# Optimization experiments

Measured on AMD Instinct MI355X. Metric: run time of the kernel, lower is better.

Reference implementation:

```python
import jax, jax.numpy as jnp
from jax import lax
import numpy as np

IN_DIM, HID, B, T = 64, 512, 256, 512


def _lstm_layer(xs, W_ih, W_hh, b_ih, b_hh):
    # xs: [B, T, D_in]; W_ih: [4H, D_in]; W_hh: [4H, H]; biases: [4H]
    Bn = xs.shape[0]
    H = W_hh.shape[1]
    # Precompute input projection for all timesteps (one big GEMM).
    x_proj = jnp.einsum('btd,gd->btg', xs, W_ih) + b_ih + b_hh  # [B, T, 4H]

    def step(carry, xp):
        h, c = carry
        g = xp + h @ W_hh.T  # [B, 4H], PyTorch gate order: i, f, g, o
        i, f, gg, o = jnp.split(g, 4, axis=-1)
        i = jax.nn.sigmoid(i)
        f = jax.nn.sigmoid(f)
        gg = jnp.tanh(gg)
        o = jax.nn.sigmoid(o)
        c = f * c + i * gg
        h = o * jnp.tanh(c)
        return (h, c), h

    z = jnp.zeros((Bn, H), xs.dtype)
    _, hs = lax.scan(step, (z, z), jnp.swapaxes(x_proj, 0, 1))  # [T, B, H]
    return jnp.swapaxes(hs, 0, 1)  # [B, T, H]


def setup_inputs() -> dict:
    key = jax.random.key(0)
    ks = jax.random.split(key, 16)
    s_in = 1.0 / np.sqrt(HID)
    u = lambda k, shp: jax.random.uniform(k, shp, jnp.float32, -s_in, s_in)
    return {
        'x': jax.random.normal(ks[0], (B, T, IN_DIM), jnp.float32),
        'W_ih0': u(ks[1], (4 * HID, IN_DIM)),
        'W_hh0': u(ks[2], (4 * HID, HID)),
        'b_ih0': u(ks[3], (4 * HID,)),
        'b_hh0': u(ks[4], (4 * HID,)),
        'W_ih1': u(ks[5], (4 * HID, HID)),
        'W_hh1': u(ks[6], (4 * HID, HID)),
        'b_ih1': u(ks[7], (4 * HID,)),
        'b_hh1': u(ks[8], (4 * HID,)),
        'W1': u(ks[9], (HID // 2, HID)),
        'b1': u(ks[10], (HID // 2,)),
        'W2': u(ks[11], (1, HID // 2)),
        'b2': u(ks[12], (1,)),
    }


def reference(x, W_ih0, W_hh0, b_ih0, b_hh0, W_ih1, W_hh1, b_ih1, b_hh1, W1, b1, W2, b2):
    h1 = _lstm_layer(x, W_ih0, W_hh0, b_ih0, b_hh0)   # [B, T, H]
    h2 = _lstm_layer(h1, W_ih1, W_hh1, b_ih1, b_hh1)  # [B, T, H] (inference: no inter-layer dropout)
    last = h2[:, -1, :]                                # final timestep
    hidden = jax.nn.relu(last @ W1.T + b1)
    return jax.nn.sigmoid(hidden @ W2.T + b2)          # [B, 1]
```

## Files before the change

### kernel.cpp

```cpp
#include <hip/hip_runtime.h>
#include <hip/hip_bf16.h>
#include <stdint.h>


#define Bsz 256
#define Tsz 512
#define IND 64
#define Hsz 512
#define BH (Bsz * Hsz)
#define FLAG_STRIDE 16

typedef __attribute__((ext_vector_type(8))) short short8;
typedef __attribute__((ext_vector_type(4))) float floatx4;

static __device__ __forceinline__ short f2bf(float f) {
    unsigned u = __float_as_uint(f);
    u += 0x7FFFu + ((u >> 16) & 1u);
    return (short)(u >> 16);
}
static __device__ __forceinline__ float bf2f(short s) {
    return __uint_as_float(((unsigned)(unsigned short)s) << 16);
}
static __device__ __forceinline__ float sigm(float z) { return 1.f / (1.f + __expf(-z)); }
static __device__ __forceinline__ float tanh_f(float z) { return 2.f / (1.f + __expf(-2.f * z)) - 1.f; }

static __device__ __forceinline__ short8 ring16(const short* p) {
    short8 v;
    asm volatile("global_load_dwordx4 %0, %1, off sc1" : "=v"(v) : "v"(p));
    return v;
}

__global__ __launch_bounds__(512, 1) void lstm_pers(
    const float* __restrict__ x,
    const float* __restrict__ Wih0, const float* __restrict__ Whh0,
    const float* __restrict__ bih0, const float* __restrict__ bhh0,
    const float* __restrict__ Wih1, const float* __restrict__ Whh1,
    const float* __restrict__ bih1, const float* __restrict__ bhh1,
    int* __restrict__ flags, short* __restrict__ h1ring, short* __restrict__ h2ring)
{
    __shared__ __align__(16) char smem[147712];
    short* w  = (short*)smem;
    float* p1 = (float*)(smem + 131072);

    const int tid = threadIdx.x;
    const int bid = blockIdx.x;
    const int layer = bid >> 7;
    const int lb    = bid & 127;
    const int grp   = lb >> 5;
    const int chunk = lb & 31;

    if (layer == 0) {
        for (int idx = tid; idx < 64 * 576; idx += 512) {
            int n = idx / 576, kc = idx - n * 576;
            int grow = (n >> 4) * Hsz + chunk * 16 + (n & 15);
            float v = (kc < IND) ? Wih0[grow * IND + kc]
                                 : Whh0[(size_t)grow * Hsz + kc - IND];
            w[n * 640 + (kc ^ ((n & 7) << 4))] = f2bf(v);
        }
    } else {
        for (int idx = tid; idx < 64 * 1024; idx += 512) {
            int n = idx >> 10, kc = idx & 1023;
            int grow = (n >> 4) * Hsz + chunk * 16 + (n & 15);
            float v = (kc < Hsz) ? Wih1[(size_t)grow * Hsz + kc]
                                 : Whh1[(size_t)grow * Hsz + kc - Hsz];
            w[n * 1024 + (kc ^ ((n & 7) << 4))] = f2bf(v);
        }
    }

    const int lane  = tid & 63;
    const int wv    = tid >> 6;
    const int mslot = wv >> 1;
    const int kh    = wv & 1;
    const int q     = lane >> 4;
    const int cl    = lane & 15;
    const int rowbase = grp * 64 + mslot * 16;
    const int hcol    = chunk * 16;

    float bI, bF, bG, bO;
    {
        const float* bi = layer ? bih1 : bih0;
        const float* bh = layer ? bhh1 : bhh0;
        int hix = hcol + cl;
        bI = bi[hix] + bh[hix];
        bF = bi[Hsz + hix] + bh[Hsz + hix];
        bG = bi[2 * Hsz + hix] + bh[2 * Hsz + hix];
        bO = bi[3 * Hsz + hix] + bh[3 * Hsz + hix];
    }

    __syncthreads();

    floatx4 c = {0.f, 0.f, 0.f, 0.f};
    const int fbase = grp * 512;

    for (int k = 0; k <= Tsz; ++k) {
        if (k > 0 && wv == 0) {
            int* fp = &flags[(fbase + k - 1) * FLAG_STRIDE];
            int spins = 0;
            while (__hip_atomic_load(fp, __ATOMIC_RELAXED, __HIP_MEMORY_SCOPE_AGENT) < 64) {
                __builtin_amdgcn_s_sleep(1);
                if (++spins > (1 << 24)) break;
            }
        }
        __syncthreads();
        asm volatile("" ::: "memory");

        const bool active = layer ? (k >= 1) : (k < Tsz);
        floatx4 acc[4];
#pragma unroll
        for (int nt = 0; nt < 4; ++nt) acc[nt] = (floatx4){0.f, 0.f, 0.f, 0.f};

        if (active) {
            if (layer == 0) {
                const short* h1p = h1ring + (size_t)((k + 1) & 1) * BH;
                const short* abase = h1p + (size_t)(rowbase + cl) * Hsz + q * 8;
                short8 af[9];
                if (kh == 0) {
#pragma unroll
                    for (int i = 2; i < 9; ++i) af[i] = ring16(abase + i * 32 - 64);
#pragma unroll
                    for (int i = 0; i < 2; ++i) {
                        const float* xp = x + ((size_t)(rowbase + cl) * Tsz + k) * IND + i * 32 + q * 8;
                        floatx4 v0 = *(const floatx4*)xp;
                        floatx4 v1 = *(const floatx4*)(xp + 4);
                        short8 av;
                        av[0] = f2bf(v0[0]); av[1] = f2bf(v0[1]); av[2] = f2bf(v0[2]); av[3] = f2bf(v0[3]);
                        av[4] = f2bf(v1[0]); av[5] = f2bf(v1[1]); av[6] = f2bf(v1[2]); av[7] = f2bf(v1[3]);
                        af[i] = av;
                    }
                } else {
#pragma unroll
                    for (int i = 0; i < 9; ++i) af[i] = ring16(abase + (9 + i) * 32 - 64);
                }
                asm volatile("s_waitcnt vmcnt(0)" ::: "memory");
                __builtin_amdgcn_sched_barrier(0);
#pragma unroll
                for (int i = 0; i < 9; ++i) {
                    const int kk = (kh * 9 + i) * 32;
#pragma unroll
                    for (int nt = 0; nt < 4; ++nt) {
                        const int n = nt * 16 + cl;
                        const int col = (kk + q * 8) ^ ((n & 7) << 4);
                        short8 bb = *(const short8*)&w[n * 640 + col];
                        acc[nt] = __builtin_amdgcn_mfma_f32_16x16x32_bf16(af[i], bb, acc[nt], 0, 0, 0);
                    }
                }
            } else {
                const short* h1p = h1ring + (size_t)((k + 1) & 1) * BH;
                const short* h2p = h2ring + (size_t)(k & 1) * BH;
                const short* src = (kh ? h2p : h1p) + (size_t)(rowbase + cl) * Hsz + q * 8;
                short8 af[16];
#pragma unroll
                for (int i = 0; i < 16; ++i) af[i] = ring16(src + i * 32);
                asm volatile("s_waitcnt vmcnt(0)" ::: "memory");
                __builtin_amdgcn_sched_barrier(0);
#pragma unroll
                for (int i = 0; i < 16; ++i) {
                    const int kk = (kh * 16 + i) * 32;
#pragma unroll
                    for (int nt = 0; nt < 4; ++nt) {
                        const int n = nt * 16 + cl;
                        const int col = (kk + q * 8) ^ ((n & 7) << 4);
                        short8 bb = *(const short8*)&w[n * 1024 + col];
                        acc[nt] = __builtin_amdgcn_mfma_f32_16x16x32_bf16(af[i], bb, acc[nt], 0, 0, 0);
                    }
                }
            }
            if (kh) {
#pragma unroll
                for (int nt = 0; nt < 4; ++nt)
#pragma unroll
                    for (int r = 0; r < 4; ++r)
                        p1[(mslot * 16 + q * 4 + r) * 65 + nt * 16 + cl] = acc[nt][r];
            }
        }

        __syncthreads();

        if (active && kh == 0) {
            short* hout = layer ? (h2ring + (size_t)((k + 1) & 1) * BH)
                                : (h1ring + (size_t)(k & 1) * BH);
#pragma unroll
            for (int r = 0; r < 4; ++r) {
                const int prow = (mslot * 16 + q * 4 + r) * 65;
                float iz = acc[0][r] + p1[prow + cl]      + bI;
                float fz = acc[1][r] + p1[prow + 16 + cl] + bF;
                float gz = acc[2][r] + p1[prow + 32 + cl] + bG;
                float oz = acc[3][r] + p1[prow + 48 + cl] + bO;
                float ii = sigm(iz);
                float ff = sigm(fz);
                float gg = tanh_f(gz);
                float oo = sigm(oz);
                float cn = ff * c[r] + ii * gg;
                c[r] = cn;
                float hv = oo * tanh_f(cn);
                __hip_atomic_store(&hout[(size_t)(rowbase + q * 4 + r) * Hsz + hcol + cl],
                                   f2bf(hv), __ATOMIC_RELAXED, __HIP_MEMORY_SCOPE_AGENT);
            }
        }

        __syncthreads();
        if (k < Tsz && tid == 0) {
            __hip_atomic_fetch_add(&flags[(fbase + k) * FLAG_STRIDE], 1,
                                   __ATOMIC_RELAXED, __HIP_MEMORY_SCOPE_AGENT);
        }
    }
}

__global__ void __launch_bounds__(256) head_kernel(
    const short* __restrict__ h2,
    const float* __restrict__ W1, const float* __restrict__ b1,
    const float* __restrict__ W2, const float* __restrict__ b2,
    float* __restrict__ out)
{
    __shared__ float hid[4][256];
    const int tid = threadIdx.x;
    const int r0 = blockIdx.x * 4;
    float acc[4] = {0.f, 0.f, 0.f, 0.f};
    const float* wrow = W1 + (size_t)tid * 512;
    for (int kk = 0; kk < 512; kk += 8) {
        float wv8[8];
#pragma unroll
        for (int j = 0; j < 8; ++j) wv8[j] = wrow[kk + j];
#pragma unroll
        for (int r = 0; r < 4; ++r) {
            short8 hv = *(const short8*)(h2 + (size_t)(r0 + r) * 512 + kk);
#pragma unroll
            for (int j = 0; j < 8; ++j) acc[r] += wv8[j] * bf2f(hv[j]);
        }
    }
#pragma unroll
    for (int r = 0; r < 4; ++r) hid[r][tid] = fmaxf(acc[r] + b1[tid], 0.f);
    __syncthreads();
    const int wv = tid >> 6, lane = tid & 63;
    float s = 0.f;
    for (int j = lane; j < 256; j += 64) s += hid[wv][j] * W2[j];
#pragma unroll
    for (int off = 32; off; off >>= 1) s += __shfl_down(s, off, 64);
    if (lane == 0) out[r0 + wv] = 1.f / (1.f + __expf(-(s + b2[0])));
}

extern "C" void kernel_launch(void* const* d_in, const int* in_sizes, int n_in,
                              void* d_out, int out_size, void* d_ws, size_t ws_size,
                              hipStream_t stream) {
    const float* x    = (const float*)d_in[0];
    const float* Wih0 = (const float*)d_in[1];
    const float* Whh0 = (const float*)d_in[2];
    const float* bih0 = (const float*)d_in[3];
    const float* bhh0 = (const float*)d_in[4];
    const float* Wih1 = (const float*)d_in[5];
    const float* Whh1 = (const float*)d_in[6];
    const float* bih1 = (const float*)d_in[7];
    const float* bhh1 = (const float*)d_in[8];
    const float* W1   = (const float*)d_in[9];
    const float* b1   = (const float*)d_in[10];
    const float* W2   = (const float*)d_in[11];
    const float* b2   = (const float*)d_in[12];
    float* out = (float*)d_out;

    const size_t FLAGS_BYTES = (size_t)4 * 512 * FLAG_STRIDE * sizeof(int);
    const size_t RING_BYTES  = (size_t)2 * Bsz * Hsz * sizeof(short);
    if (ws_size < FLAGS_BYTES + 2 * RING_BYTES) return;

    char* ws = (char*)d_ws;
    int*   flags  = (int*)ws;
    short* h1ring = (short*)(ws + FLAGS_BYTES);
    short* h2ring = (short*)(ws + FLAGS_BYTES + RING_BYTES);

    hipMemsetAsync(d_ws, 0, FLAGS_BYTES + 2 * RING_BYTES, stream);

    void* args[] = {
        (void*)&x,
        (void*)&Wih0, (void*)&Whh0, (void*)&bih0, (void*)&bhh0,
        (void*)&Wih1, (void*)&Whh1, (void*)&bih1, (void*)&bhh1,
        (void*)&flags, (void*)&h1ring, (void*)&h2ring
    };
    hipLaunchCooperativeKernel((const void*)lstm_pers, dim3(256), dim3(512), args, 0, stream);

    const short* h2last = h2ring + (size_t)Bsz * Hsz;
    head_kernel<<<dim3(64), dim3(256), 0, stream>>>(h2last, W1, b1, W2, b2, out);
}
```

Measured before the change: 4.856 ms.

## Replace per-step atomic counters with per-block monotonic slots polled per lane

The per-timestep fetch_add counters (64 arrivals per group, one flag per step) become a 64-slot array per group. Each block stores its latest completed step and every wave polls the slots in parallel, one lane per slot, which drops atomic RMW contention and the block-wide barrier after the wait. The x-input load and bf16 conversion are hoisted ahead of the spin so they overlap the wait, and the LDS partial-sum stride changes from 65 to 66. The risk is that visibility of the slot store relative to the h ring writes now relies on relaxed ordering.

```diff
diff --git a/kernel.cpp b/kernel.cpp
--- a/kernel.cpp
+++ b/kernel.cpp
@@ -8,7 +8,7 @@
 #define IND 64
 #define Hsz 512
 #define BH (Bsz * Hsz)
-#define FLAG_STRIDE 16
+#define P1S 66
 
 typedef __attribute__((ext_vector_type(8))) short short8;
 typedef __attribute__((ext_vector_type(4))) float floatx4;
@@ -36,9 +36,9 @@
     const float* __restrict__ bih0, const float* __restrict__ bhh0,
     const float* __restrict__ Wih1, const float* __restrict__ Whh1,
     const float* __restrict__ bih1, const float* __restrict__ bhh1,
-    int* __restrict__ flags, short* __restrict__ h1ring, short* __restrict__ h2ring)
+    int* __restrict__ slots, short* __restrict__ h1ring, short* __restrict__ h2ring)
 {
-    __shared__ __align__(16) char smem[147712];
+    __shared__ __align__(16) char smem[131072 + 64 * P1S * 4];
     short* w  = (short*)smem;
     float* p1 = (float*)(smem + 131072);
 
@@ -48,6 +48,7 @@
     const int lb    = bid & 127;
     const int grp   = lb >> 5;
     const int chunk = lb & 31;
+    const int sid   = layer * 32 + chunk;
 
     if (layer == 0) {
         for (int idx = tid; idx < 64 * 576; idx += 512) {
@@ -90,21 +91,36 @@
     __syncthreads();
 
     floatx4 c = {0.f, 0.f, 0.f, 0.f};
-    const int fbase = grp * 512;
+    const int* myslots = &slots[grp * 64 + lane];
 
     for (int k = 0; k <= Tsz; ++k) {
-        if (k > 0 && wv == 0) {
-            int* fp = &flags[(fbase + k - 1) * FLAG_STRIDE];
+        const bool active = layer ? (k >= 1) : (k < Tsz);
+        short8 af[16];
+
+        if (active && layer == 0 && kh == 0) {
+#pragma unroll
+            for (int i = 0; i < 2; ++i) {
+                const float* xp = x + ((size_t)(rowbase + cl) * Tsz + k) * IND + i * 32 + q * 8;
+                floatx4 v0 = *(const floatx4*)xp;
+                floatx4 v1 = *(const floatx4*)(xp + 4);
+                short8 av;
+                av[0] = f2bf(v0[0]); av[1] = f2bf(v0[1]); av[2] = f2bf(v0[2]); av[3] = f2bf(v0[3]);
+                av[4] = f2bf(v1[0]); av[5] = f2bf(v1[1]); av[6] = f2bf(v1[2]); av[7] = f2bf(v1[3]);
+                af[i] = av;
+            }
+        }
+
+        if (k > 0) {
+            int v = __hip_atomic_load(myslots, __ATOMIC_RELAXED, __HIP_MEMORY_SCOPE_AGENT);
             int spins = 0;
-            while (__hip_atomic_load(fp, __ATOMIC_RELAXED, __HIP_MEMORY_SCOPE_AGENT) < 64) {
+            while (v < k) {
                 __builtin_amdgcn_s_sleep(1);
-                if (++spins > (1 << 24)) break;
-            }
-        }
-        __syncthreads();
-        asm volatile("" ::: "memory");
-
-        const bool active = layer ? (k >= 1) : (k < Tsz);
+                v = __hip_atomic_load(myslots, __ATOMIC_RELAXED, __HIP_MEMORY_SCOPE_AGENT);
+                if (++spins > (1 << 22)) break;
+            }
+            asm volatile("" ::: "memory");
+        }
+
         floatx4 acc[4];
 #pragma unroll
         for (int nt = 0; nt < 4; ++nt) acc[nt] = (floatx4){0.f, 0.f, 0.f, 0.f};
@@ -113,20 +129,9 @@
             if (layer == 0) {
                 const short* h1p = h1ring + (size_t)((k + 1) & 1) * BH;
                 const short* abase = h1p + (size_t)(rowbase + cl) * Hsz + q * 8;
-                short8 af[9];
                 if (kh == 0) {
 #pragma unroll
                     for (int i = 2; i < 9; ++i) af[i] = ring16(abase + i * 32 - 64);
-#pragma unroll
-                    for (int i = 0; i < 2; ++i) {
-                        const float* xp = x + ((size_t)(rowbase + cl) * Tsz + k) * IND + i * 32 + q * 8;
-                        floatx4 v0 = *(const floatx4*)xp;
-                        floatx4 v1 = *(const floatx4*)(xp + 4);
-                        short8 av;
-                        av[0] = f2bf(v0[0]); av[1] = f2bf(v0[1]); av[2] = f2bf(v0[2]); av[3] = f2bf(v0[3]);
-                        av[4] = f2bf(v1[0]); av[5] = f2bf(v1[1]); av[6] = f2bf(v1[2]); av[7] = f2bf(v1[3]);
-                        af[i] = av;
-                    }
                 } else {
 #pragma unroll
                     for (int i = 0; i < 9; ++i) af[i] = ring16(abase + (9 + i) * 32 - 64);
@@ -148,7 +153,6 @@
                 const short* h1p = h1ring + (size_t)((k + 1) & 1) * BH;
                 const short* h2p = h2ring + (size_t)(k & 1) * BH;
                 const short* src = (kh ? h2p : h1p) + (size_t)(rowbase + cl) * Hsz + q * 8;
-                short8 af[16];
 #pragma unroll
                 for (int i = 0; i < 16; ++i) af[i] = ring16(src + i * 32);
                 asm volatile("s_waitcnt vmcnt(0)" ::: "memory");
@@ -170,7 +174,7 @@
                 for (int nt = 0; nt < 4; ++nt)
 #pragma unroll
                     for (int r = 0; r < 4; ++r)
-                        p1[(mslot * 16 + q * 4 + r) * 65 + nt * 16 + cl] = acc[nt][r];
+                        p1[(mslot * 16 + q * 4 + r) * P1S + nt * 16 + cl] = acc[nt][r];
             }
         }
 
@@ -181,7 +185,7 @@
                                 : (h1ring + (size_t)(k & 1) * BH);
 #pragma unroll
             for (int r = 0; r < 4; ++r) {
-                const int prow = (mslot * 16 + q * 4 + r) * 65;
+                const int prow = (mslot * 16 + q * 4 + r) * P1S;
                 float iz = acc[0][r] + p1[prow + cl]      + bI;
                 float fz = acc[1][r] + p1[prow + 16 + cl] + bF;
                 float gz = acc[2][r] + p1[prow + 32 + cl] + bG;
@@ -200,8 +204,8 @@
 
         __syncthreads();
         if (k < Tsz && tid == 0) {
-            __hip_atomic_fetch_add(&flags[(fbase + k) * FLAG_STRIDE], 1,
-                                   __ATOMIC_RELAXED, __HIP_MEMORY_SCOPE_AGENT);
+            __hip_atomic_store(&slots[grp * 64 + sid], k + 1,
+                               __ATOMIC_RELAXED, __HIP_MEMORY_SCOPE_AGENT);
         }
     }
 }
@@ -257,22 +261,22 @@
     const float* b2   = (const float*)d_in[12];
     float* out = (float*)d_out;
 
-    const size_t FLAGS_BYTES = (size_t)4 * 512 * FLAG_STRIDE * sizeof(int);
+    const size_t SLOTS_BYTES = (size_t)4 * 64 * sizeof(int);
     const size_t RING_BYTES  = (size_t)2 * Bsz * Hsz * sizeof(short);
-    if (ws_size < FLAGS_BYTES + 2 * RING_BYTES) return;
+    if (ws_size < SLOTS_BYTES + 2 * RING_BYTES) return;
 
     char* ws = (char*)d_ws;
-    int*   flags  = (int*)ws;
-    short* h1ring = (short*)(ws + FLAGS_BYTES);
-    short* h2ring = (short*)(ws + FLAGS_BYTES + RING_BYTES);
-
-    hipMemsetAsync(d_ws, 0, FLAGS_BYTES + 2 * RING_BYTES, stream);
+    int*   slots  = (int*)ws;
+    short* h1ring = (short*)(ws + SLOTS_BYTES);
+    short* h2ring = (short*)(ws + SLOTS_BYTES + RING_BYTES);
+
+    hipMemsetAsync(d_ws, 0, SLOTS_BYTES + 2 * RING_BYTES, stream);
 
     void* args[] = {
         (void*)&x,
         (void*)&Wih0, (void*)&Whh0, (void*)&bih0, (void*)&bhh0,
         (void*)&Wih1, (void*)&Whh1, (void*)&bih1, (void*)&bhh1,
-        (void*)&flags, (void*)&h1ring, (void*)&h2ring
+        (void*)&slots, (void*)&h1ring, (void*)&h2ring
     };
     hipLaunchCooperativeKernel((const void*)lstm_pers, dim3(256), dim3(512), args, 0, stream);
 
```

Measured after the change: 4.807 ms. About the same (-1.0%).
